# Optimization experiments

Hardware: AMD Instinct MI355X
Metric: run time of the kernel (lower is better)

The kernel has to match this reference:

```python
import jax, jax.numpy as jnp
import numpy as np
from jax import lax

B, T = 4, 2048
IN_CH, SKIP_CH, OUT_CH, K = 256, 128, 128, 5
N_MAMBA, D_STATE, D_CONV, EXPAND = 2, 16, 4, 2
D_INNER = EXPAND * OUT_CH
DT_RANK = (OUT_CH + 15) // 16  # ceil(d_model/16) = 8
L = 2 * T
EPS = 1e-5


def setup_inputs() -> dict:
    key = jax.random.key(0)
    ks = jax.random.split(key, 16)
    def rn(k, shape, s=0.02):
        return jax.random.normal(k, shape, jnp.float32) * s
    A_init = jnp.broadcast_to(jnp.arange(1, D_STATE + 1, dtype=jnp.float32),
                              (N_MAMBA, 2, D_INNER, D_STATE))
    return {
        'x': rn(ks[0], (B, IN_CH, T), 1.0),
        'skip': rn(ks[1], (B, SKIP_CH, L), 1.0),
        'up_w': rn(ks[2], (IN_CH, IN_CH, K)),       # torch ConvTranspose1d weight (in,out,k)
        'up_b': jnp.zeros((IN_CH,), jnp.float32),
        'fus_w': rn(ks[3], (OUT_CH, IN_CH + SKIP_CH)),  # 1x1 conv
        'fus_b': jnp.zeros((OUT_CH,), jnp.float32),
        'gn_w': jnp.ones((OUT_CH,), jnp.float32),
        'gn_b': jnp.zeros((OUT_CH,), jnp.float32),
        'prelu_a': jnp.array(0.25, jnp.float32),
        'ln_w': jnp.ones((N_MAMBA, OUT_CH), jnp.float32),
        'ln_b': jnp.zeros((N_MAMBA, OUT_CH), jnp.float32),
        'in_w': rn(ks[4], (N_MAMBA, 2, 2 * D_INNER, OUT_CH)),
        'conv_w': rn(ks[5], (N_MAMBA, 2, D_INNER, D_CONV), 0.1),
        'conv_b': jnp.zeros((N_MAMBA, 2, D_INNER), jnp.float32),
        'xproj_w': rn(ks[6], (N_MAMBA, 2, DT_RANK + 2 * D_STATE, D_INNER)),
        'dtproj_w': rn(ks[7], (N_MAMBA, 2, D_INNER, DT_RANK), 0.1),
        'dtproj_b': rn(ks[8], (N_MAMBA, 2, D_INNER), 0.1),
        'A_log': jnp.log(A_init),
        'Dp': jnp.ones((N_MAMBA, 2, D_INNER), jnp.float32),
        'out_w': rn(ks[9], (N_MAMBA, 2, OUT_CH, D_INNER)),
    }


def _mamba_branch(xn, cw, cb, iw, xw, dw, db, Alog, Dp, ow):
    # xn: [B, L, d_model] -> [B, L, d_model]; standard Mamba selective scan.
    xz = jnp.einsum('bld,ed->ble', xn, iw)            # [B,L,2*D_INNER]
    xi, z = jnp.split(xz, 2, axis=-1)
    # causal depthwise conv over time
    xc = lax.conv_general_dilated(xi.transpose(0, 2, 1), cw[:, None, :], (1,),
                                  [(D_CONV - 1, 0)], feature_group_count=D_INNER,
                                  dimension_numbers=('NCH', 'OIH', 'NCH'))
    xi = jax.nn.silu(xc + cb[None, :, None]).transpose(0, 2, 1)  # [B,L,D_INNER]
    dbl = jnp.einsum('bld,ed->ble', xi, xw)           # [B,L,DT_RANK+2N]
    dt = jax.nn.softplus(jnp.einsum('blr,dr->bld', dbl[..., :DT_RANK], dw) + db)
    Bc = dbl[..., DT_RANK:DT_RANK + D_STATE]          # [B,L,N]
    Cc = dbl[..., DT_RANK + D_STATE:]                 # [B,L,N]
    A = -jnp.exp(Alog)                                # [D_INNER,N]
    dA = jnp.exp(dt[..., None] * A)                   # [B,L,D_INNER,N]
    dBx = dt[..., None] * Bc[:, :, None, :] * xi[..., None]
    def comb(c1, c2):
        a1, b1 = c1
        a2, b2 = c2
        return a1 * a2, a2 * b1 + b2
    _, h = lax.associative_scan(comb, (dA, dBx), axis=1)  # h_t = dA_t h_{t-1} + dBx_t
    y = jnp.einsum('bldn,bln->bld', h, Cc) + Dp * xi
    return jnp.einsum('ble,de->bld', y * jax.nn.silu(z), ow)


def _forward(x, skip, up_w, up_b, fus_w, fus_b, gn_w, gn_b, prelu_a, ln_w, ln_b,
             in_w, conv_w, conv_b, xproj_w, dtproj_w, dtproj_b, A_log, Dp, out_w):
    p = K // 2
    # ConvTranspose1d(stride=2, padding=p, output_padding=1) == lhs-dilated conv with flipped kernel
    wt = jnp.flip(up_w, -1).transpose(1, 0, 2)        # (out,in,k)
    u = lax.conv_general_dilated(x, wt, (1,), [(K - 1 - p, K - 1 - p + 1)],
                                 lhs_dilation=(2,),
                                 dimension_numbers=('NCH', 'OIH', 'NCH'))
    u = u + up_b[None, :, None]
    u = u[..., :skip.shape[-1]]
    h = jnp.concatenate([u, skip], axis=1)            # [B, in+skip, L]
    h = jnp.einsum('bct,oc->bot', h, fus_w) + fus_b[None, :, None]
    # GroupNorm(1, C): normalize over (C,T) per sample
    mu = h.mean(axis=(1, 2), keepdims=True)
    var = h.var(axis=(1, 2), keepdims=True)
    h = (h - mu) / jnp.sqrt(var + EPS) * gn_w[None, :, None] + gn_b[None, :, None]
    h = jnp.where(h >= 0, h, prelu_a * h)             # PReLU (single param)
    h = h.transpose(0, 2, 1)                          # [B, L, C]
    for i in range(N_MAMBA):
        # BiMambaBlock: pre-LN, forward + time-reversed Mamba, residual sum
        mu2 = h.mean(-1, keepdims=True)
        v2 = h.var(-1, keepdims=True)
        xn = (h - mu2) / jnp.sqrt(v2 + EPS) * ln_w[i] + ln_b[i]
        f = _mamba_branch(xn, conv_w[i, 0], conv_b[i, 0], in_w[i, 0], xproj_w[i, 0],
                          dtproj_w[i, 0], dtproj_b[i, 0], A_log[i, 0], Dp[i, 0], out_w[i, 0])
        b = _mamba_branch(jnp.flip(xn, 1), conv_w[i, 1], conv_b[i, 1], in_w[i, 1], xproj_w[i, 1],
                          dtproj_w[i, 1], dtproj_b[i, 1], A_log[i, 1], Dp[i, 1], out_w[i, 1])
        h = h + f + jnp.flip(b, 1)
    return h.transpose(0, 2, 1)                       # [B, C_out, L]


def reference(x, skip, up_w, up_b, fus_w, fus_b, gn_w, gn_b, prelu_a, ln_w, ln_b,
              in_w, conv_w, conv_b, xproj_w, dtproj_w, dtproj_b, A_log, Dp, out_w):
    return _forward(x, skip, up_w, up_b, fus_w, fus_b, gn_w, gn_b, prelu_a, ln_w, ln_b,
                    in_w, conv_w, conv_b, xproj_w, dtproj_w, dtproj_b, A_log, Dp, out_w)
```

## Files before the change

### kernel.cpp

```cpp
#include <hip/hip_runtime.h>
#include <hip/hip_bf16.h>

#define Bsz 4
#define Tt 2048
#define Ll 4096
#define NC 128
#define CH 32

typedef short bf16x8 __attribute__((ext_vector_type(8)));
typedef float f32x4 __attribute__((ext_vector_type(4)));

static __device__ __forceinline__ float bs2f(unsigned short u){
  union{float f; unsigned int i;} v; v.i = ((unsigned int)u)<<16; return v.f;
}
static __device__ __forceinline__ unsigned short f2bs(float f){
  union{float f; unsigned int i;} v; v.f = f;
  unsigned int r = (v.i + 0x7fffu + ((v.i>>16)&1u)) >> 16;
  return (unsigned short)r;
}

__global__ void k_cvt(const float* __restrict__ src, unsigned short* __restrict__ dst, int n){
  int i = blockIdx.x*256 + threadIdx.x;
  if (i < n) dst[i] = f2bs(src[i]);
}

__global__ void k_prepx(const float* __restrict__ xw, unsigned short* __restrict__ wxb){
  int row = blockIdx.x, br = blockIdx.y, col = threadIdx.x;
  float v = (row < 40) ? xw[((size_t)br*40 + row)*256 + col] : 0.f;
  wxb[((size_t)br*64 + row)*256 + col] = f2bs(v);
}

__global__ void k_compose(const float* __restrict__ up_w, const float* __restrict__ fus_w,
                          const float* __restrict__ fus_b, const float* __restrict__ up_b,
                          unsigned short* __restrict__ WEb, unsigned short* __restrict__ WOb,
                          unsigned short* __restrict__ FWSb, float* __restrict__ BIAS2){
  int i = blockIdx.x;
  int o = threadIdx.x;
  float a0=0.f,a1=0.f,a2=0.f,a3=0.f,a4=0.f;
  for (int c=0;c<256;c++){
    float f = fus_w[o*384+c];
    const float* w = up_w + ((size_t)i*256+c)*5;
    a0 += f*w[0]; a1 += f*w[1]; a2 += f*w[2];
    a3 += f*w[3]; a4 += f*w[4];
  }
  WEb[(size_t)o*768 +       i] = f2bs(a4);
  WEb[(size_t)o*768 + 256 + i] = f2bs(a2);
  WEb[(size_t)o*768 + 512 + i] = f2bs(a0);
  WOb[(size_t)o*512 +       i] = f2bs(a3);
  WOb[(size_t)o*512 + 256 + i] = f2bs(a1);
  if (i<128) FWSb[o*128 + i] = f2bs(fus_w[o*384+256+i]);
  if (i==0){
    float bb = fus_b[o];
    for (int c=0;c<256;c++) bb += fus_w[o*384+c]*up_b[c];
    BIAS2[o]=bb;
  }
}

__global__ __launch_bounds__(256) void k_tx(const float* __restrict__ x, unsigned short* __restrict__ XT){
  __shared__ float tile[64][65];
  int b=blockIdx.z, t0=blockIdx.x*64, i0=blockIdx.y*64;
  int tid=threadIdx.x;
  for (int it=0;it<16;it++){
    int idx=it*256+tid; int ii=idx>>6, tt=idx&63;
    tile[ii][tt] = x[((size_t)b*256+i0+ii)*Tt + t0+tt];
  }
  __syncthreads();
  for (int it=0;it<16;it++){
    int idx=it*256+tid; int tt=idx>>6, ii=idx&63;
    XT[((size_t)b*2050 + t0+tt+1)*256 + i0+ii] = f2bs(tile[ii][tt]);
  }
}

__global__ void k_zero(unsigned short* __restrict__ XT){
  int tid=threadIdx.x;
  for (int b=0;b<Bsz;b++){
    XT[((size_t)b*2050)*256 + tid] = 0;
    XT[((size_t)b*2050+2049)*256 + tid] = 0;
  }
}

__global__ __launch_bounds__(256) void k_ts(const float* __restrict__ skip, unsigned short* __restrict__ SKT){
  __shared__ float tile[64][65];
  int b=blockIdx.z, l0=blockIdx.x*64, s0=blockIdx.y*64;
  int tid=threadIdx.x;
  for (int it=0;it<16;it++){
    int idx=it*256+tid; int ss=idx>>6, ll=idx&63;
    tile[ss][ll] = skip[((size_t)b*128+s0+ss)*Ll + l0+ll];
  }
  __syncthreads();
  for (int it=0;it<16;it++){
    int idx=it*256+tid; int ll=idx>>6, ss=idx&63;
    SKT[((size_t)b*Ll + l0+ll)*128 + s0+ss] = f2bs(tile[ss][ll]);
  }
}

__global__ __launch_bounds__(256) void k_up(const unsigned short* __restrict__ XT,
                     const unsigned short* __restrict__ SKT,
                     const unsigned short* __restrict__ WEb, const unsigned short* __restrict__ WOb,
                     const unsigned short* __restrict__ FWSb, const float* __restrict__ B2,
                     float* __restrict__ h0, float* __restrict__ gst){
  __shared__ unsigned short XL[66*264];
  __shared__ unsigned short Wb[128*72];
  __shared__ float red0[256], red1[256];
  int bt = blockIdx.x, par = blockIdx.y, b = blockIdx.z;
  int t0 = bt*64;
  int tid = threadIdx.x;
  int wave = tid>>6, lane = tid&63;
  int wm = wave>>1, wn = wave&1;
  int quad = lane>>4, l16 = lane&15;

  for (int idx=tid; idx<66*32; idx+=256){
    int row = idx>>5, c8 = idx&31;
    *(uint4*)&XL[row*264 + c8*8] = *(const uint4*)&XT[((size_t)b*2050 + t0 + row)*256 + c8*8];
  }

  const unsigned short* Wsrc = par ? WOb : WEb;
  const int Kw = par ? 512 : 768;
  const int tapbase = par ? 1 : 0;
  f32x4 acc[2][4];
  #pragma unroll
  for (int i=0;i<2;i++)
    #pragma unroll
    for (int j=0;j<4;j++) acc[i][j] = (f32x4){0.f,0.f,0.f,0.f};

  int nch = Kw>>6;
  for (int kc=0; kc<nch; kc++){
    __syncthreads();
    #pragma unroll
    for (int it=0; it<4; it++){
      int idx = it*256+tid;
      int row = idx>>3, c8 = idx&7;
      *(uint4*)&Wb[row*72 + c8*8] = *(const uint4*)&Wsrc[(size_t)row*Kw + kc*64 + c8*8];
    }
    __syncthreads();
    #pragma unroll
    for (int ks=0; ks<64; ks+=32){
      int kg = kc*64 + ks;
      int tap = kg>>8, ib = kg&255;
      bf16x8 af[2], bf[4];
      #pragma unroll
      for (int mt=0;mt<2;mt++)
        af[mt] = *(bf16x8*)&XL[(wm*32+mt*16+l16 + tapbase + tap)*264 + ib + quad*8];
      #pragma unroll
      for (int nt=0;nt<4;nt++)
        bf[nt] = *(bf16x8*)&Wb[(wn*64+nt*16+l16)*72 + ks + quad*8];
      #pragma unroll
      for (int mt=0;mt<2;mt++)
        #pragma unroll
        for (int nt=0;nt<4;nt++)
          acc[mt][nt] = __builtin_amdgcn_mfma_f32_16x16x32_bf16(af[mt], bf[nt], acc[mt][nt], 0,0,0);
    }
  }

  __syncthreads();
  for (int idx=tid; idx<64*16; idx+=256){
    int row = idx>>4, c8 = idx&15;
    *(uint4*)&XL[row*136 + c8*8] = *(const uint4*)&SKT[((size_t)b*Ll + 2*(t0+row)+par)*128 + c8*8];
  }
  for (int kc=0; kc<2; kc++){
    __syncthreads();
    #pragma unroll
    for (int it=0; it<4; it++){
      int idx = it*256+tid;
      int row = idx>>3, c8 = idx&7;
      *(uint4*)&Wb[row*72 + c8*8] = *(const uint4*)&FWSb[(size_t)row*128 + kc*64 + c8*8];
    }
    __syncthreads();
    #pragma unroll
    for (int ks=0; ks<64; ks+=32){
      bf16x8 af[2], bf[4];
      #pragma unroll
      for (int mt=0;mt<2;mt++)
        af[mt] = *(bf16x8*)&XL[(wm*32+mt*16+l16)*136 + kc*64 + ks + quad*8];
      #pragma unroll
      for (int nt=0;nt<4;nt++)
        bf[nt] = *(bf16x8*)&Wb[(wn*64+nt*16+l16)*72 + ks + quad*8];
      #pragma unroll
      for (int mt=0;mt<2;mt++)
        #pragma unroll
        for (int nt=0;nt<4;nt++)
          acc[mt][nt] = __builtin_amdgcn_mfma_f32_16x16x32_bf16(af[mt], bf[nt], acc[mt][nt], 0,0,0);
    }
  }

  float s1=0.f, s2=0.f;
  #pragma unroll
  for (int mt=0;mt<2;mt++)
    #pragma unroll
    for (int nt=0;nt<4;nt++)
      #pragma unroll
      for (int r=0;r<4;r++){
        int m = wm*32 + mt*16 + quad*4 + r;
        int lrow = 2*(t0+m) + par;
        int col = wn*64 + nt*16 + l16;
        float v = acc[mt][nt][r] + B2[col];
        h0[((size_t)b*Ll + lrow)*128 + col] = v;
        s1 += v; s2 += v*v;
      }
  red0[tid]=s1; red1[tid]=s2;
  __syncthreads();
  for (int st=128; st>0; st>>=1){
    if (tid<st){ red0[tid]+=red0[tid+st]; red1[tid]+=red1[tid+st]; }
    __syncthreads();
  }
  if (tid==0){ atomicAdd(&gst[b*2], red0[0]); atomicAdd(&gst[b*2+1], red1[0]); }
}

__global__ void k_gnfin(float* gst){
  int b = threadIdx.x;
  if (b < Bsz){
    float n = (float)Ll*128.f;
    float mu = gst[b*2]/n;
    float var = gst[b*2+1]/n - mu*mu;
    gst[8+b]=mu; gst[12+b]=rsqrtf(var+1e-5f);
  }
}

__global__ __launch_bounds__(256) void k_gnln(const float* __restrict__ h0, const float* __restrict__ gn_w,
                      const float* __restrict__ gn_b, const float* __restrict__ pa,
                      const float* __restrict__ gst, const float* __restrict__ lnw,
                      const float* __restrict__ lnb, float* __restrict__ hres,
                      unsigned short* __restrict__ xn){
  int row = blockIdx.x*4 + (threadIdx.x>>6);
  int lane = threadIdx.x & 63;
  int b = row >> 12;
  float mu_g = gst[8+b], inv_g = gst[12+b];
  float a = pa[0];
  const float* hp = h0 + (size_t)row*128;
  float u0 = (hp[lane]   -mu_g)*inv_g*gn_w[lane]    + gn_b[lane];
  float u1 = (hp[lane+64]-mu_g)*inv_g*gn_w[lane+64] + gn_b[lane+64];
  float v0 = u0>=0.f ? u0 : a*u0;
  float v1 = u1>=0.f ? u1 : a*u1;
  float* rp = hres + (size_t)row*128;
  rp[lane] = v0; rp[lane+64] = v1;
  float s = v0+v1, q = v0*v0+v1*v1;
  #pragma unroll
  for (int off=32; off>0; off>>=1){
    s += __shfl_xor(s, off, 64);
    q += __shfl_xor(q, off, 64);
  }
  float mu = s*(1.f/128.f);
  float rs = rsqrtf(q*(1.f/128.f)-mu*mu + 1e-5f);
  unsigned short* xp = xn + (size_t)row*128;
  xp[lane]    = f2bs((v0-mu)*rs*lnw[lane]    + lnb[lane]);
  xp[lane+64] = f2bs((v1-mu)*rs*lnw[lane+64] + lnb[lane+64]);
}

__global__ __launch_bounds__(256) void k_ln(const float* __restrict__ hres, const float* __restrict__ lnw,
                     const float* __restrict__ lnb, unsigned short* __restrict__ xn){
  int row = blockIdx.x*4 + (threadIdx.x>>6);
  int lane = threadIdx.x & 63;
  const float* hp = hres + (size_t)row*128;
  float v0 = hp[lane], v1 = hp[lane+64];
  float s = v0+v1, q = v0*v0+v1*v1;
  #pragma unroll
  for (int off=32; off>0; off>>=1){
    s += __shfl_xor(s, off, 64);
    q += __shfl_xor(q, off, 64);
  }
  float mu = s*(1.f/128.f);
  float rs = rsqrtf(q*(1.f/128.f)-mu*mu + 1e-5f);
  unsigned short* xp = xn + (size_t)row*128;
  xp[lane]    = f2bs((v0-mu)*rs*lnw[lane]    + lnb[lane]);
  xp[lane+64] = f2bs((v1-mu)*rs*lnw[lane+64] + lnb[lane+64]);
}

__global__ __launch_bounds__(256) void k_gemm_in(const unsigned short* __restrict__ A,
                          const unsigned short* __restrict__ W,
                          unsigned short* __restrict__ C){
  __shared__ unsigned short As[128*72];
  __shared__ unsigned short Bs[128*72];
  int tid = threadIdx.x;
  int row0 = blockIdx.x*128;
  int n0   = blockIdx.y*128;
  int dir  = blockIdx.z;
  const unsigned short* Wp = W + (size_t)dir*512*128;
  unsigned short* Cp = C + (size_t)dir*Bsz*Ll*512;
  int wave = tid>>6, lane = tid&63;
  int wm = wave>>1, wn = wave&1;
  int quad = lane>>4, l16 = lane&15;
  f32x4 acc[4][4];
  #pragma unroll
  for (int i=0;i<4;i++)
    #pragma unroll
    for (int j=0;j<4;j++) acc[i][j] = (f32x4){0.f,0.f,0.f,0.f};

  for (int kb=0; kb<128; kb+=64){
    __syncthreads();
    #pragma unroll
    for (int it=0; it<4; it++){
      int idx = it*256 + tid;
      int row = idx>>3, c8 = idx&7;
      int r = row0 + row;
      int p = r & (Ll-1); int bb = r >> 12;
      int src = (bb<<12) + (dir ? (Ll-1-p) : p);
      *(uint4*)&As[row*72 + c8*8] = *(const uint4*)&A[(size_t)src*128 + kb + c8*8];
      *(uint4*)&Bs[row*72 + c8*8] = *(const uint4*)&Wp[(size_t)(n0+row)*128 + kb + c8*8];
    }
    __syncthreads();
    #pragma unroll
    for (int ks=0; ks<64; ks+=32){
      bf16x8 af[4], bf[4];
      #pragma unroll
      for (int mt=0;mt<4;mt++)
        af[mt] = *(bf16x8*)&As[(wm*64+mt*16+l16)*72 + ks + quad*8];
      #pragma unroll
      for (int nt=0;nt<4;nt++)
        bf[nt] = *(bf16x8*)&Bs[(wn*64+nt*16+l16)*72 + ks + quad*8];
      #pragma unroll
      for (int mt=0;mt<4;mt++)
        #pragma unroll
        for (int nt=0;nt<4;nt++)
          acc[mt][nt] = __builtin_amdgcn_mfma_f32_16x16x32_bf16(af[mt], bf[nt], acc[mt][nt], 0,0,0);
    }
  }
  #pragma unroll
  for (int mt=0;mt<4;mt++)
    #pragma unroll
    for (int nt=0;nt<4;nt++)
      #pragma unroll
      for (int r=0;r<4;r++){
        int row = row0 + wm*64 + mt*16 + quad*4 + r;
        int col = n0 + wn*64 + nt*16 + l16;
        Cp[(size_t)row*512 + col] = f2bs(acc[mt][nt][r]);
      }
}

__global__ __launch_bounds__(256) void k_gemm_out(const unsigned short* __restrict__ Y,
                           const unsigned short* __restrict__ W,
                           float* __restrict__ C){
  __shared__ unsigned short As[64*72];
  __shared__ unsigned short Bs[128*72];
  int tid = threadIdx.x;
  int row0 = blockIdx.x*64;
  int wave = tid>>6, lane = tid&63;
  int wm = wave>>1, wn = wave&1;
  int quad = lane>>4, l16 = lane&15;
  const size_t planeY = (size_t)Bsz*Ll*256;
  f32x4 acc[2][4];
  #pragma unroll
  for (int i=0;i<2;i++)
    #pragma unroll
    for (int j=0;j<4;j++) acc[i][j] = (f32x4){0.f,0.f,0.f,0.f};

  for (int kc=0; kc<8; kc++){
    int dirp = kc>>2;
    int kb = (kc&3)*64;
    const unsigned short* Wp = W + (size_t)dirp*128*256;
    __syncthreads();
    #pragma unroll
    for (int it=0; it<2; it++){
      int idx = it*256 + tid;
      int row = idx>>3, c8 = idx&7;
      int r = row0 + row;
      int p = r & (Ll-1); int bb = r >> 12;
      int srow = dirp ? ((bb<<12) + (Ll-1-p)) : r;
      *(uint4*)&As[row*72 + c8*8] = *(const uint4*)&Y[dirp*planeY + (size_t)srow*256 + kb + c8*8];
    }
    #pragma unroll
    for (int it=0; it<4; it++){
      int idx = it*256 + tid;
      int row = idx>>3, c8 = idx&7;
      *(uint4*)&Bs[row*72 + c8*8] = *(const uint4*)&Wp[(size_t)row*256 + kb + c8*8];
    }
    __syncthreads();
    #pragma unroll
    for (int ks=0; ks<64; ks+=32){
      bf16x8 af[2], bf[4];
      #pragma unroll
      for (int mt=0;mt<2;mt++)
        af[mt] = *(bf16x8*)&As[(wm*32+mt*16+l16)*72 + ks + quad*8];
      #pragma unroll
      for (int nt=0;nt<4;nt++)
        bf[nt] = *(bf16x8*)&Bs[(wn*64+nt*16+l16)*72 + ks + quad*8];
      #pragma unroll
      for (int mt=0;mt<2;mt++)
        #pragma unroll
        for (int nt=0;nt<4;nt++)
          acc[mt][nt] = __builtin_amdgcn_mfma_f32_16x16x32_bf16(af[mt], bf[nt], acc[mt][nt], 0,0,0);
    }
  }
  #pragma unroll
  for (int mt=0;mt<2;mt++)
    #pragma unroll
    for (int nt=0;nt<4;nt++)
      #pragma unroll
      for (int r=0;r<4;r++){
        int row = row0 + wm*32 + mt*16 + quad*4 + r;
        int col = wn*64 + nt*16 + l16;
        C[(size_t)row*128 + col] += acc[mt][nt][r];
      }
}

__global__ __launch_bounds__(256) void k_xproj3(const unsigned short* __restrict__ xz,
                        const unsigned short* __restrict__ wxb,
                        const float* __restrict__ cw, const float* __restrict__ cb,
                        unsigned short* __restrict__ xib, float* __restrict__ dbl){
  __shared__ unsigned short xiS[64*264];
  __shared__ unsigned short Bs[64*72];
  int tid = threadIdx.x;
  int dir = blockIdx.y;
  xz  += (size_t)dir*Bsz*Ll*512;
  wxb += (size_t)dir*64*256;
  cw  += dir*1024;
  cb  += dir*256;
  xib += (size_t)dir*Bsz*Ll*256;
  dbl += (size_t)dir*Bsz*Ll*40;
  size_t row0 = (size_t)blockIdx.x*64;
  int p0 = (int)(row0 & (Ll-1));

  {
    int d = tid;
    float4 w4 = *(const float4*)&cw[d*4];
    float bias = cb[d];
    float w0, w1, w2;
    if (p0 == 0){ w0=0.f; w1=0.f; w2=0.f; }
    else {
      w0 = bs2f(xz[(row0-3)*512 + d]);
      w1 = bs2f(xz[(row0-2)*512 + d]);
      w2 = bs2f(xz[(row0-1)*512 + d]);
    }
    #pragma unroll 4
    for (int rr=0; rr<64; rr++){
      float xv = bs2f(xz[(row0+rr)*512 + d]);
      float acc = bias + w4.x*w0 + w4.y*w1 + w4.z*w2 + w4.w*xv;
      float v = acc/(1.f+__expf(-acc));
      unsigned short us = f2bs(v);
      xiS[rr*264 + d] = us;
      xib[(row0+rr)*256 + d] = us;
      w0=w1; w1=w2; w2=xv;
    }
  }

  int wave = tid>>6, lane = tid&63;
  int quad = lane>>4, l16 = lane&15;
  f32x4 acc[4];
  #pragma unroll
  for (int j=0;j<4;j++) acc[j] = (f32x4){0.f,0.f,0.f,0.f};

  for (int kb=0; kb<256; kb+=64){
    __syncthreads();
    #pragma unroll
    for (int it=0; it<2; it++){
      int idx = it*256 + tid;
      int row = idx>>3, c8 = idx&7;
      *(uint4*)&Bs[row*72 + c8*8] = *(const uint4*)&wxb[(size_t)row*256 + kb + c8*8];
    }
    __syncthreads();
    #pragma unroll
    for (int ks=0; ks<64; ks+=32){
      bf16x8 af = *(bf16x8*)&xiS[(wave*16+l16)*264 + kb + ks + quad*8];
      #pragma unroll
      for (int nt=0;nt<4;nt++){
        bf16x8 bf = *(bf16x8*)&Bs[(nt*16+l16)*72 + ks + quad*8];
        acc[nt] = __builtin_amdgcn_mfma_f32_16x16x32_bf16(af, bf, acc[nt], 0,0,0);
      }
    }
  }
  #pragma unroll
  for (int nt=0;nt<4;nt++)
    #pragma unroll
    for (int r=0;r<4;r++){
      int m = wave*16 + quad*4 + r;
      int col = nt*16 + l16;
      if (col < 40) dbl[(row0+m)*40 + col] = acc[nt][r];
    }
}

#define POWTREE(e1, pw) { \
  float e2 = (e1)*(e1); float e4 = e2*e2; float e8 = e4*e4; \
  pw[0]=(e1); pw[1]=e2; pw[2]=e2*(e1); pw[3]=e4; pw[4]=e4*(e1); pw[5]=e4*e2; \
  pw[6]=e4*pw[2]; pw[7]=e8; pw[8]=e8*(e1); pw[9]=e8*e2; pw[10]=e8*pw[2]; \
  pw[11]=e8*e4; pw[12]=e8*pw[4]; pw[13]=e8*pw[5]; pw[14]=e8*pw[6]; pw[15]=e8*e8; }

__global__ __launch_bounds__(256) void k_scan1(const float* __restrict__ dbl,
                       const unsigned short* __restrict__ xib, const float* __restrict__ Alog,
                       const float* __restrict__ dtw, const float* __restrict__ dtb,
                       float* __restrict__ P, float* __restrict__ Q){
  __shared__ float dblS[CH*24];
  int b = blockIdx.y, c = blockIdx.x, dir = blockIdx.z;
  int d = threadIdx.x;
  const float* dblP = dbl + (size_t)dir*Bsz*Ll*40;
  const unsigned short* xiP = xib + (size_t)dir*Bsz*Ll*256;
  size_t base = (size_t)b*Ll + (size_t)c*CH;
  if (d < CH*6){
    int p = d/6, j = d - p*6;
    *(float4*)&dblS[p*24 + j*4] = *(const float4*)&dblP[(base+p)*40 + j*4];
  }
  float A[16];
  #pragma unroll
  for (int j=0;j<4;j++){
    float4 a4 = *(const float4*)&Alog[(size_t)dir*4096 + d*16 + j*4];
    A[4*j]=-__expf(a4.x); A[4*j+1]=-__expf(a4.y); A[4*j+2]=-__expf(a4.z); A[4*j+3]=-__expf(a4.w);
  }
  bool chain = true;
  #pragma unroll
  for (int n=1;n<16;n++){
    float expect = A[0]*(float)(n+1);
    if (fabsf(A[n]-expect) > 1e-3f*fabsf(expect)) chain = false;
  }
  float wv[8];
  {
    const float* dw = dtw + (size_t)dir*2048 + d*8;
    float4 w0 = *(const float4*)&dw[0];
    float4 w1 = *(const float4*)&dw[4];
    wv[0]=w0.x; wv[1]=w0.y; wv[2]=w0.z; wv[3]=w0.w;
    wv[4]=w1.x; wv[5]=w1.y; wv[6]=w1.z; wv[7]=w1.w;
  }
  float bbt = dtb[dir*256 + d];
  __syncthreads();
  float h[16], pr[16];
  #pragma unroll
  for (int n=0;n<16;n++){ h[n]=0.f; pr[n]=1.f; }
  const unsigned short* xip = xiP + base*256 + d;
  if (chain){
    float A0 = A[0];
    float sdt = 0.f;
    #pragma unroll 2
    for (int p=0;p<CH;p++){
      const float* rw = &dblS[p*24];
      float4 t0 = *(const float4*)&rw[0], t1 = *(const float4*)&rw[4];
      float a0 = bbt + t0.x*wv[0]+t0.y*wv[1]+t0.z*wv[2]+t0.w*wv[3]
                     + t1.x*wv[4]+t1.y*wv[5]+t1.z*wv[6]+t1.w*wv[7];
      float dtv = (a0>20.f)? a0 : __logf(1.f+__expf(a0));
      float xiv = bs2f(xip[(size_t)p*256]);
      float dx = dtv*xiv;
      sdt += dtv;
      float pw[16];
      float e1 = __expf(dtv*A0);
      POWTREE(e1, pw);
      float bc[16];
      *(float4*)&bc[0]  = *(const float4*)&rw[8];
      *(float4*)&bc[4]  = *(const float4*)&rw[12];
      *(float4*)&bc[8]  = *(const float4*)&rw[16];
      *(float4*)&bc[12] = *(const float4*)&rw[20];
      #pragma unroll
      for (int n=0;n<16;n++) h[n] = pw[n]*h[n] + bc[n]*dx;
    }
    float E = __expf(A0*sdt);
    POWTREE(E, pr);
  } else {
    for (int p=0;p<CH;p++){
      const float* rw = &dblS[p*24];
      float4 t0 = *(const float4*)&rw[0], t1 = *(const float4*)&rw[4];
      float a0 = bbt + t0.x*wv[0]+t0.y*wv[1]+t0.z*wv[2]+t0.w*wv[3]
                     + t1.x*wv[4]+t1.y*wv[5]+t1.z*wv[6]+t1.w*wv[7];
      float dtv = (a0>20.f)? a0 : __logf(1.f+__expf(a0));
      float xiv = bs2f(xip[(size_t)p*256]);
      float dx = dtv*xiv;
      float bc[16];
      *(float4*)&bc[0]  = *(const float4*)&rw[8];
      *(float4*)&bc[4]  = *(const float4*)&rw[12];
      *(float4*)&bc[8]  = *(const float4*)&rw[16];
      *(float4*)&bc[12] = *(const float4*)&rw[20];
      #pragma unroll
      for (int n=0;n<16;n++){
        float a = __expf(dtv*A[n]);
        h[n] = a*h[n] + bc[n]*dx;
        pr[n] *= a;
      }
    }
  }
  size_t sbase = (size_t)dir*Bsz*NC*4096 + ((size_t)(b*NC + c))*4096 + d*16;
  #pragma unroll
  for (int j=0;j<4;j++){
    *(float4*)&P[sbase + 4*j] = (float4){pr[4*j],pr[4*j+1],pr[4*j+2],pr[4*j+3]};
    *(float4*)&Q[sbase + 4*j] = (float4){h[4*j],h[4*j+1],h[4*j+2],h[4*j+3]};
  }
}

__global__ __launch_bounds__(64) void k_scan2(const float* __restrict__ P, float* __restrict__ Q){
  int b = blockIdx.y, dir = blockIdx.z;
  int dn4 = (blockIdx.x*64 + threadIdx.x)*4;
  size_t plane = (size_t)dir*Bsz*NC*4096;
  float4 H = {0.f,0.f,0.f,0.f};
  for (int c=0;c<NC;c++){
    size_t idx = plane + ((size_t)(b*NC + c))*4096 + dn4;
    float4 p = *(const float4*)&P[idx];
    float4 q = *(const float4*)&Q[idx];
    *(float4*)&Q[idx] = H;
    H.x = p.x*H.x + q.x; H.y = p.y*H.y + q.y;
    H.z = p.z*H.z + q.z; H.w = p.w*H.w + q.w;
  }
}

__global__ __launch_bounds__(256) void k_scan3(const float* __restrict__ dbl,
                       unsigned short* xiy, const float* __restrict__ Alog,
                       const float* __restrict__ dtw, const float* __restrict__ dtb,
                       const float* __restrict__ Dpw, const float* __restrict__ Hs,
                       const unsigned short* __restrict__ xz){
  __shared__ float dblS[CH*40];
  int b = blockIdx.y, c = blockIdx.x, dir = blockIdx.z;
  int d = threadIdx.x;
  const float* dblP = dbl + (size_t)dir*Bsz*Ll*40;
  unsigned short* xiP = xiy + (size_t)dir*Bsz*Ll*256;
  const unsigned short* xzP = xz + (size_t)dir*Bsz*Ll*512;
  size_t base = (size_t)b*Ll + (size_t)c*CH;
  for (int idx=d; idx<CH*10; idx+=256){
    int p = idx/10, j = idx - p*10;
    *(float4*)&dblS[p*40 + j*4] = *(const float4*)&dblP[(base+p)*40 + j*4];
  }
  float A[16];
  #pragma unroll
  for (int j=0;j<4;j++){
    float4 a4 = *(const float4*)&Alog[(size_t)dir*4096 + d*16 + j*4];
    A[4*j]=-__expf(a4.x); A[4*j+1]=-__expf(a4.y); A[4*j+2]=-__expf(a4.z); A[4*j+3]=-__expf(a4.w);
  }
  bool chain = true;
  #pragma unroll
  for (int n=1;n<16;n++){
    float expect = A[0]*(float)(n+1);
    if (fabsf(A[n]-expect) > 1e-3f*fabsf(expect)) chain = false;
  }
  float wv[8];
  {
    const float* dw = dtw + (size_t)dir*2048 + d*8;
    float4 w0 = *(const float4*)&dw[0];
    float4 w1 = *(const float4*)&dw[4];
    wv[0]=w0.x; wv[1]=w0.y; wv[2]=w0.z; wv[3]=w0.w;
    wv[4]=w1.x; wv[5]=w1.y; wv[6]=w1.z; wv[7]=w1.w;
  }
  float bbt = dtb[dir*256 + d];
  float Dp = Dpw[dir*256 + d];
  float h[16];
  size_t sbase = (size_t)dir*Bsz*NC*4096 + ((size_t)(b*NC + c))*4096 + d*16;
  #pragma unroll
  for (int j=0;j<4;j++){
    float4 h4 = *(const float4*)&Hs[sbase + 4*j];
    h[4*j]=h4.x; h[4*j+1]=h4.y; h[4*j+2]=h4.z; h[4*j+3]=h4.w;
  }
  __syncthreads();
  unsigned short* xip = xiP + base*256 + d;
  const unsigned short* zp = xzP + base*512 + 256 + d;
  if (chain){
    float A0 = A[0];
    #pragma unroll 2
    for (int p=0;p<CH;p++){
      const float* rw = &dblS[p*40];
      float4 t0 = *(const float4*)&rw[0], t1 = *(const float4*)&rw[4];
      float a0 = bbt + t0.x*wv[0]+t0.y*wv[1]+t0.z*wv[2]+t0.w*wv[3]
                     + t1.x*wv[4]+t1.y*wv[5]+t1.z*wv[6]+t1.w*wv[7];
      float dtv = (a0>20.f)? a0 : __logf(1.f+__expf(a0));
      float xiv = bs2f(xip[(size_t)p*256]);
      float dx = dtv*xiv;
      float pw[16];
      float e1 = __expf(dtv*A0);
      POWTREE(e1, pw);
      float bc[16], cc[16];
      *(float4*)&bc[0]  = *(const float4*)&rw[8];
      *(float4*)&bc[4]  = *(const float4*)&rw[12];
      *(float4*)&bc[8]  = *(const float4*)&rw[16];
      *(float4*)&bc[12] = *(const float4*)&rw[20];
      *(float4*)&cc[0]  = *(const float4*)&rw[24];
      *(float4*)&cc[4]  = *(const float4*)&rw[28];
      *(float4*)&cc[8]  = *(const float4*)&rw[32];
      *(float4*)&cc[12] = *(const float4*)&rw[36];
      float acc = 0.f;
      #pragma unroll
      for (int n=0;n<16;n++){
        h[n] = pw[n]*h[n] + bc[n]*dx;
        acc += h[n]*cc[n];
      }
      float z = bs2f(zp[(size_t)p*512]);
      float g = z/(1.f+__expf(-z));
      xip[(size_t)p*256] = f2bs((acc + Dp*xiv)*g);
    }
  } else {
    for (int p=0;p<CH;p++){
      const float* rw = &dblS[p*40];
      float4 t0 = *(const float4*)&rw[0], t1 = *(const float4*)&rw[4];
      float a0 = bbt + t0.x*wv[0]+t0.y*wv[1]+t0.z*wv[2]+t0.w*wv[3]
                     + t1.x*wv[4]+t1.y*wv[5]+t1.z*wv[6]+t1.w*wv[7];
      float dtv = (a0>20.f)? a0 : __logf(1.f+__expf(a0));
      float xiv = bs2f(xip[(size_t)p*256]);
      float dx = dtv*xiv;
      float bc[16], cc[16];
      *(float4*)&bc[0]  = *(const float4*)&rw[8];
      *(float4*)&bc[4]  = *(const float4*)&rw[12];
      *(float4*)&bc[8]  = *(const float4*)&rw[16];
      *(float4*)&bc[12] = *(const float4*)&rw[20];
      *(float4*)&cc[0]  = *(const float4*)&rw[24];
      *(float4*)&cc[4]  = *(const float4*)&rw[28];
      *(float4*)&cc[8]  = *(const float4*)&rw[32];
      *(float4*)&cc[12] = *(const float4*)&rw[36];
      float acc = 0.f;
      #pragma unroll
      for (int n=0;n<16;n++){
        float a = __expf(dtv*A[n]);
        h[n] = a*h[n] + bc[n]*dx;
        acc += h[n]*cc[n];
      }
      float z = bs2f(zp[(size_t)p*512]);
      float g = z/(1.f+__expf(-z));
      xip[(size_t)p*256] = f2bs((acc + Dp*xiv)*g);
    }
  }
}

__global__ __launch_bounds__(256) void k_final(const float* __restrict__ hres, float* __restrict__ out){
  __shared__ float tile[64*129];
  int b = blockIdx.y, l0 = blockIdx.x*64;
  int tid = threadIdx.x;
  for (int q=0;q<32;q++){
    int idx = q*256 + tid;
    int l = idx >> 7, c = idx & 127;
    tile[l*129 + c] = hres[((size_t)b*Ll + l0 + l)*128 + c];
  }
  __syncthreads();
  int lo = tid & 63; int cbase = tid >> 6;
  for (int q=0;q<32;q++){
    int c = cbase + q*4;
    out[((size_t)b*128 + c)*Ll + l0 + lo] = tile[lo*129 + c];
  }
}

extern "C" void kernel_launch(void* const* d_in, const int* in_sizes, int n_in,
                              void* d_out, int out_size, void* d_ws, size_t ws_size,
                              hipStream_t stream){
  const float* x      = (const float*)d_in[0];
  const float* skip   = (const float*)d_in[1];
  const float* up_w   = (const float*)d_in[2];
  const float* up_b   = (const float*)d_in[3];
  const float* fus_w  = (const float*)d_in[4];
  const float* fus_b  = (const float*)d_in[5];
  const float* gn_w   = (const float*)d_in[6];
  const float* gn_b   = (const float*)d_in[7];
  const float* pa     = (const float*)d_in[8];
  const float* ln_w   = (const float*)d_in[9];
  const float* ln_b   = (const float*)d_in[10];
  const float* in_w   = (const float*)d_in[11];
  const float* conv_w = (const float*)d_in[12];
  const float* conv_b = (const float*)d_in[13];
  const float* xproj_w= (const float*)d_in[14];
  const float* dtproj_w=(const float*)d_in[15];
  const float* dtproj_b=(const float*)d_in[16];
  const float* A_log  = (const float*)d_in[17];
  const float* Dp     = (const float*)d_in[18];
  const float* out_w  = (const float*)d_in[19];

  float* w = (float*)d_ws;
  size_t off=0;
  float* B2 = w+off; off += 128;
  float* GST= w+off; off += 16;
  off = (off+3)&~(size_t)3;
  float* HR = w+off; off += (size_t)Bsz*Ll*128;
  float* DBL2= w+off; off += 2*(size_t)Bsz*Ll*40;
  unsigned short* XNB = (unsigned short*)(w+off); off += (size_t)Bsz*Ll*128/2;
  unsigned short* XZB2= (unsigned short*)(w+off); off += 2*(size_t)Bsz*Ll*512/2;
  unsigned short* IWB = (unsigned short*)(w+off); off += 2*2*512*128/2;
  unsigned short* OWB = (unsigned short*)(w+off); off += 2*2*128*256/2;
  unsigned short* WXB = (unsigned short*)(w+off); off += 2*2*64*256/2;
  unsigned short* WEb = (unsigned short*)(w+off); off += 768*128/2;
  unsigned short* WOb = (unsigned short*)(w+off); off += 512*128/2;
  unsigned short* FWSb= (unsigned short*)(w+off); off += 128*128/2;
  size_t planeS = (size_t)Bsz*NC*4096;
  float* U1 = w+off; off += 4*planeS;
  unsigned short* XT  = (unsigned short*)U1;
  unsigned short* SKT = (unsigned short*)(U1 + 1049604);
  float* SP = U1;
  float* SQ = U1 + 2*planeS;
  float* U2 = w+off; off += 2*(size_t)Bsz*Ll*128;
  float* H0 = U2;
  unsigned short* XIB2 = (unsigned short*)U2;

  hipMemsetAsync(GST, 0, 16*sizeof(float), stream);
  k_cvt<<<(2*2*512*128+255)/256,256,0,stream>>>(in_w, IWB, 2*2*512*128);
  k_cvt<<<(2*2*128*256+255)/256,256,0,stream>>>(out_w, OWB, 2*2*128*256);
  k_prepx<<<dim3(64,4),256,0,stream>>>(xproj_w, WXB);
  k_compose<<<256,128,0,stream>>>(up_w, fus_w, fus_b, up_b, WEb, WOb, FWSb, B2);
  k_tx<<<dim3(Tt/64, 4, Bsz),256,0,stream>>>(x, XT);
  k_zero<<<1,256,0,stream>>>(XT);
  k_ts<<<dim3(Ll/64, 2, Bsz),256,0,stream>>>(skip, SKT);
  k_up<<<dim3(32, 2, Bsz),256,0,stream>>>(XT, SKT, WEb, WOb, FWSb, B2, H0, GST);
  k_gnfin<<<1,64,0,stream>>>(GST);
  k_gnln<<<Bsz*Ll/4,256,0,stream>>>(H0, gn_w, gn_b, pa, GST, ln_w, ln_b, HR, XNB);
  for (int i=0;i<2;i++){
    if (i==1) k_ln<<<Bsz*Ll/4,256,0,stream>>>(HR, ln_w + 128, ln_b + 128, XNB);
    k_gemm_in<<<dim3(128,4,2),256,0,stream>>>(XNB, IWB + (size_t)(i*2)*512*128, XZB2);
    k_xproj3<<<dim3(Bsz*Ll/64,2),256,0,stream>>>(XZB2, WXB + (size_t)(i*2)*64*256,
                                                 conv_w + (i*2)*1024, conv_b + (i*2)*256,
                                                 XIB2, DBL2);
    k_scan1<<<dim3(NC,Bsz,2),256,0,stream>>>(DBL2, XIB2, A_log + (i*2)*4096,
                                             dtproj_w + (i*2)*2048, dtproj_b + (i*2)*256, SP, SQ);
    k_scan2<<<dim3(16,Bsz,2),64,0,stream>>>(SP, SQ);
    k_scan3<<<dim3(NC,Bsz,2),256,0,stream>>>(DBL2, XIB2, A_log + (i*2)*4096,
                                             dtproj_w + (i*2)*2048, dtproj_b + (i*2)*256,
                                             Dp + (i*2)*256, SQ, XZB2);
    k_gemm_out<<<256,256,0,stream>>>(XIB2, OWB + (size_t)(i*2)*128*256, HR);
  }
  k_final<<<dim3(Ll/64,Bsz),256,0,stream>>>(HR, (float*)d_out);
}
```

Before: 440.5 us.

## Halve scan chunk size and pass dt sums instead of decay products

The chunk length drops from 32 to 16 steps, doubling the number of chunks so the per-chunk scan kernels launch more blocks. Chunk-level decay products are no longer stored per state. scan1 writes only the sum of dt per channel, and scan2 rebuilds exp(A*sum_dt) from A_log and prefetches the next chunk's values. This removes one full P plane of memory traffic and reuses the XNB buffer for the dt sums. In exchange, the sequential chunk loop in scan2 becomes twice as long and computes exponentials inline.

```diff
diff --git a/kernel.cpp b/kernel.cpp
--- a/kernel.cpp
+++ b/kernel.cpp
@@ -4,8 +4,8 @@
 #define Bsz 4
 #define Tt 2048
 #define Ll 4096
-#define NC 128
-#define CH 32
+#define NC 256
+#define CH 16
 
 typedef short bf16x8 __attribute__((ext_vector_type(8)));
 typedef float f32x4 __attribute__((ext_vector_type(4)));
@@ -476,7 +476,7 @@
 __global__ __launch_bounds__(256) void k_scan1(const float* __restrict__ dbl,
                        const unsigned short* __restrict__ xib, const float* __restrict__ Alog,
                        const float* __restrict__ dtw, const float* __restrict__ dtb,
-                       float* __restrict__ P, float* __restrict__ Q){
+                       float* __restrict__ SD, float* __restrict__ Q){
   __shared__ float dblS[CH*24];
   int b = blockIdx.y, c = blockIdx.x, dir = blockIdx.z;
   int d = threadIdx.x;
@@ -509,13 +509,13 @@
   }
   float bbt = dtb[dir*256 + d];
   __syncthreads();
-  float h[16], pr[16];
-  #pragma unroll
-  for (int n=0;n<16;n++){ h[n]=0.f; pr[n]=1.f; }
+  float h[16];
+  #pragma unroll
+  for (int n=0;n<16;n++) h[n]=0.f;
+  float sdt = 0.f;
   const unsigned short* xip = xiP + base*256 + d;
   if (chain){
     float A0 = A[0];
-    float sdt = 0.f;
     #pragma unroll 2
     for (int p=0;p<CH;p++){
       const float* rw = &dblS[p*24];
@@ -537,8 +537,6 @@
       #pragma unroll
       for (int n=0;n<16;n++) h[n] = pw[n]*h[n] + bc[n]*dx;
     }
-    float E = __expf(A0*sdt);
-    POWTREE(E, pr);
   } else {
     for (int p=0;p<CH;p++){
       const float* rw = &dblS[p*24];
@@ -548,6 +546,7 @@
       float dtv = (a0>20.f)? a0 : __logf(1.f+__expf(a0));
       float xiv = bs2f(xip[(size_t)p*256]);
       float dx = dtv*xiv;
+      sdt += dtv;
       float bc[16];
       *(float4*)&bc[0]  = *(const float4*)&rw[8];
       *(float4*)&bc[4]  = *(const float4*)&rw[12];
@@ -557,30 +556,45 @@
       for (int n=0;n<16;n++){
         float a = __expf(dtv*A[n]);
         h[n] = a*h[n] + bc[n]*dx;
-        pr[n] *= a;
       }
     }
   }
-  size_t sbase = (size_t)dir*Bsz*NC*4096 + ((size_t)(b*NC + c))*4096 + d*16;
-  #pragma unroll
-  for (int j=0;j<4;j++){
-    *(float4*)&P[sbase + 4*j] = (float4){pr[4*j],pr[4*j+1],pr[4*j+2],pr[4*j+3]};
+  SD[(((size_t)dir*Bsz + b)*NC + c)*256 + d] = sdt;
+  size_t sbase = (size_t)dir*Bsz*NC*4096 + ((size_t)(b*NC + c))*4096 + (size_t)d*16;
+  #pragma unroll
+  for (int j=0;j<4;j++)
     *(float4*)&Q[sbase + 4*j] = (float4){h[4*j],h[4*j+1],h[4*j+2],h[4*j+3]};
-  }
-}
-
-__global__ __launch_bounds__(64) void k_scan2(const float* __restrict__ P, float* __restrict__ Q){
+}
+
+__global__ __launch_bounds__(64) void k_scan2(const float* __restrict__ SD, float* __restrict__ Q,
+                                              const float* __restrict__ Alog){
   int b = blockIdx.y, dir = blockIdx.z;
-  int dn4 = (blockIdx.x*64 + threadIdx.x)*4;
-  size_t plane = (size_t)dir*Bsz*NC*4096;
+  int t = blockIdx.x*64 + threadIdx.x;
+  int dn4 = t*4;
+  int d = dn4 >> 4;
+  float4 A4;
+  {
+    const float* ap = Alog + (size_t)dir*4096 + dn4;
+    A4.x = -__expf(ap[0]); A4.y = -__expf(ap[1]);
+    A4.z = -__expf(ap[2]); A4.w = -__expf(ap[3]);
+  }
+  const float* sd = SD + (((size_t)dir*Bsz + b)*NC)*256 + d;
+  float* q = Q + (size_t)dir*Bsz*NC*4096 + (size_t)b*NC*4096 + dn4;
   float4 H = {0.f,0.f,0.f,0.f};
+  float  s_n = sd[0];
+  float4 q_n = *(const float4*)q;
   for (int c=0;c<NC;c++){
-    size_t idx = plane + ((size_t)(b*NC + c))*4096 + dn4;
-    float4 p = *(const float4*)&P[idx];
-    float4 q = *(const float4*)&Q[idx];
-    *(float4*)&Q[idx] = H;
-    H.x = p.x*H.x + q.x; H.y = p.y*H.y + q.y;
-    H.z = p.z*H.z + q.z; H.w = p.w*H.w + q.w;
+    float s_c = s_n; float4 q_c = q_n;
+    if (c+1 < NC){
+      s_n = sd[(size_t)(c+1)*256];
+      q_n = *(const float4*)(q + (size_t)(c+1)*4096);
+    }
+    float4 p;
+    p.x = __expf(A4.x*s_c); p.y = __expf(A4.y*s_c);
+    p.z = __expf(A4.z*s_c); p.w = __expf(A4.w*s_c);
+    *(float4*)(q + (size_t)c*4096) = H;
+    H.x = p.x*H.x + q_c.x; H.y = p.y*H.y + q_c.y;
+    H.z = p.z*H.z + q_c.z; H.w = p.w*H.w + q_c.w;
   }
 }
 
@@ -623,7 +637,7 @@
   float bbt = dtb[dir*256 + d];
   float Dp = Dpw[dir*256 + d];
   float h[16];
-  size_t sbase = (size_t)dir*Bsz*NC*4096 + ((size_t)(b*NC + c))*4096 + d*16;
+  size_t sbase = (size_t)dir*Bsz*NC*4096 + ((size_t)(b*NC + c))*4096 + (size_t)d*16;
   #pragma unroll
   for (int j=0;j<4;j++){
     float4 h4 = *(const float4*)&Hs[sbase + 4*j];
@@ -754,11 +768,11 @@
   unsigned short* WOb = (unsigned short*)(w+off); off += 512*128/2;
   unsigned short* FWSb= (unsigned short*)(w+off); off += 128*128/2;
   size_t planeS = (size_t)Bsz*NC*4096;
-  float* U1 = w+off; off += 4*planeS;
+  float* U1 = w+off; off += 2*planeS;
   unsigned short* XT  = (unsigned short*)U1;
   unsigned short* SKT = (unsigned short*)(U1 + 1049604);
-  float* SP = U1;
-  float* SQ = U1 + 2*planeS;
+  float* SQ = U1;
+  float* SD = (float*)XNB;
   float* U2 = w+off; off += 2*(size_t)Bsz*Ll*128;
   float* H0 = U2;
   unsigned short* XIB2 = (unsigned short*)U2;
@@ -781,8 +795,8 @@
                                                  conv_w + (i*2)*1024, conv_b + (i*2)*256,
                                                  XIB2, DBL2);
     k_scan1<<<dim3(NC,Bsz,2),256,0,stream>>>(DBL2, XIB2, A_log + (i*2)*4096,
-                                             dtproj_w + (i*2)*2048, dtproj_b + (i*2)*256, SP, SQ);
-    k_scan2<<<dim3(16,Bsz,2),64,0,stream>>>(SP, SQ);
+                                             dtproj_w + (i*2)*2048, dtproj_b + (i*2)*256, SD, SQ);
+    k_scan2<<<dim3(16,Bsz,2),64,0,stream>>>(SD, SQ, A_log + (i*2)*4096);
     k_scan3<<<dim3(NC,Bsz,2),256,0,stream>>>(DBL2, XIB2, A_log + (i*2)*4096,
                                              dtproj_w + (i*2)*2048, dtproj_b + (i*2)*256,
                                              Dp + (i*2)*256, SQ, XZB2);
```

Result: no change. 436.8 us (-0.8%).
